# Kernel optimization log

Hardware: AMD Instinct MI355X
Metric: run time of the kernel (lower is better)

## Reference

```python
import jax, jax.numpy as jnp
import numpy as np

BIG = 1000000.0


def setup_inputs() -> dict:
    key = jax.random.key(0)
    k1, k2 = jax.random.split(key)
    embeddings = jax.random.normal(k1, (8192, 128), dtype=jnp.float32)
    labels = jax.random.randint(k2, (8192,), 0, 512, dtype=jnp.int64)
    return {"embeddings": embeddings, "labels": labels, "margin": jnp.float32(0.5)}


def _pairwise_euclidean(x):
    # [N, N] Euclidean distance matrix, numerically safe sqrt (zero diag)
    sq = jnp.sum(x * x, axis=1)
    d2 = sq[:, None] + sq[None, :] - 2.0 * (x @ x.T)
    d2 = jnp.maximum(d2, 0.0)
    nz = d2 > 0.0
    return jnp.where(nz, jnp.sqrt(jnp.where(nz, d2, 1.0)), 0.0)


def reference(embeddings, labels, margin):
    n = embeddings.shape[0]
    dist = _pairwise_euclidean(embeddings)                      # [N, N]
    same = (labels[:, None] == labels[None, :]).astype(dist.dtype)
    mask_pos = same - jnp.eye(n, dtype=dist.dtype)              # positives, excl. self
    mask_neg = 1.0 - same                                       # different label
    pos_dist = jnp.max(dist * mask_pos, axis=1)                 # hardest positive
    neg_dist = jnp.min(dist + (1.0 - mask_neg) * BIG, axis=1)   # hardest negative
    loss = jax.nn.relu(pos_dist - neg_dist + margin)
    return jnp.mean(loss)
```

## Files before the change

### kernel.cpp

```cpp
#include <hip/hip_runtime.h>
#include <hip/hip_bf16.h>

#define NROW 8192
#define DIM  128
#define BI   128
#define BJ   128
#define JSPLIT 8
#define LSTR 136
#define BIGF 1e30f

typedef __attribute__((ext_vector_type(8))) short bf16x8;
typedef __attribute__((ext_vector_type(4))) float f32x4;


__device__ __forceinline__ unsigned short f2bf(float f) {
    unsigned u = __float_as_uint(f);
    unsigned r = (u + 0x7fffu + ((u >> 16) & 1u)) >> 16;
    return (unsigned short)r;
}

__global__ __launch_bounds__(256) void prep_kernel(const float* __restrict__ x,
                                                   unsigned short* __restrict__ xb,
                                                   float* __restrict__ sq,
                                                   unsigned* __restrict__ posb,
                                                   unsigned* __restrict__ negb,
                                                   float* __restrict__ out) {
    int gtid = blockIdx.x * 256 + threadIdx.x;
    if (gtid < NROW) {
        posb[gtid] = 0u;
        negb[gtid] = __float_as_uint(BIGF);
    }
    if (gtid == 0) out[0] = 0.0f;
    int row  = gtid >> 6;
    int lane = threadIdx.x & 63;
    const float* xr = x + (size_t)row * DIM;
    float a = xr[lane];
    float b = xr[lane + 64];
    xb[(size_t)row * DIM + lane]      = f2bf(a);
    xb[(size_t)row * DIM + lane + 64] = f2bf(b);
    float s = a * a + b * b;
    #pragma unroll
    for (int o = 32; o > 0; o >>= 1) s += __shfl_down(s, o);
    if (lane == 0) sq[row] = s;
}

__global__ __launch_bounds__(256, 2) void tri_mfma(const unsigned short* __restrict__ xb,
                                                   const int* __restrict__ lbl,
                                                   const float* __restrict__ sq,
                                                   unsigned* __restrict__ posb,
                                                   unsigned* __restrict__ negb) {
    __shared__ unsigned short As[BI * LSTR];
    __shared__ unsigned short Bs[BJ * LSTR];

    const int bid = blockIdx.x;
    const int rb  = bid >> 3;
    const int jq  = bid & 7;
    const int i0  = rb * BI;
    const int t    = threadIdx.x;
    const int lane = t & 63;
    const int w    = t >> 6;
    const int wrow = (w >> 1) * 64;
    const int wcol = (w & 1) * 64;
    const int quad = lane >> 4;
    const int l15  = lane & 15;

    {
        const int srow = t >> 4;
        const int schk = t & 15;
        #pragma unroll
        for (int it = 0; it < 8; it++) {
            int row = srow + it * 16;
            uint4 v = *(const uint4*)(xb + (size_t)(i0 + row) * DIM + schk * 8);
            *(uint4*)(&As[row * LSTR + schk * 8]) = v;
        }
    }

    float sqi[4][4];
    int   lbli[4][4];
    #pragma unroll
    for (int ti = 0; ti < 4; ti++) {
        int rbase = i0 + wrow + ti * 16 + quad * 4;
        float4 s4 = *(const float4*)(sq + rbase);
        int4   l4 = *(const int4*)(lbl + rbase);
        sqi[ti][0] = s4.x; sqi[ti][1] = s4.y; sqi[ti][2] = s4.z; sqi[ti][3] = s4.w;
        lbli[ti][0] = l4.x; lbli[ti][1] = l4.y; lbli[ti][2] = l4.z; lbli[ti][3] = l4.w;
    }

    float posm[4][4], negm[4][4];
    #pragma unroll
    for (int ti = 0; ti < 4; ti++)
        #pragma unroll
        for (int r = 0; r < 4; r++) { posm[ti][r] = -BIGF; negm[ti][r] = BIGF; }

    #pragma unroll 1
    for (int jt = 0; jt < (NROW / JSPLIT) / BJ; jt++) {
        const int j0 = jq * (NROW / JSPLIT) + jt * BJ;
        __syncthreads();
        {
            const int srow = t >> 4;
            const int schk = t & 15;
            #pragma unroll
            for (int it = 0; it < 8; it++) {
                int row = srow + it * 16;
                uint4 v = *(const uint4*)(xb + (size_t)(j0 + row) * DIM + schk * 8);
                *(uint4*)(&Bs[row * LSTR + schk * 8]) = v;
            }
        }
        __syncthreads();

        float sqj[4]; int lblj[4];
        #pragma unroll
        for (int tj = 0; tj < 4; tj++) {
            int c = j0 + wcol + tj * 16 + l15;
            sqj[tj]  = sq[c];
            lblj[tj] = lbl[c];
        }

        f32x4 acc[4][4];
        #pragma unroll
        for (int ti = 0; ti < 4; ti++)
            #pragma unroll
            for (int tj = 0; tj < 4; tj++) acc[ti][tj] = (f32x4){0.f, 0.f, 0.f, 0.f};

        #pragma unroll
        for (int ks = 0; ks < 4; ks++) {
            bf16x8 af[4], bfr[4];
            #pragma unroll
            for (int ti = 0; ti < 4; ti++)
                af[ti] = *(const bf16x8*)(&As[(wrow + ti * 16 + l15) * LSTR + ks * 32 + quad * 8]);
            #pragma unroll
            for (int tj = 0; tj < 4; tj++)
                bfr[tj] = *(const bf16x8*)(&Bs[(wcol + tj * 16 + l15) * LSTR + ks * 32 + quad * 8]);
            #pragma unroll
            for (int ti = 0; ti < 4; ti++)
                #pragma unroll
                for (int tj = 0; tj < 4; tj++)
                    acc[ti][tj] = __builtin_amdgcn_mfma_f32_16x16x32_bf16(af[ti], bfr[tj], acc[ti][tj], 0, 0, 0);
        }

        const bool diag = (i0 + wrow) == (j0 + wcol);
        #pragma unroll
        for (int ti = 0; ti < 4; ti++)
            #pragma unroll
            for (int tj = 0; tj < 4; tj++)
                #pragma unroll
                for (int r = 0; r < 4; r++) {
                    float s = fmaf(-2.0f, acc[ti][tj][r], sqj[tj]);
                    bool same = (lbli[ti][r] == lblj[tj]);
                    bool isd  = diag && (ti == tj) && (quad * 4 + r == l15);
                    float sp = (same && !isd) ? s : -BIGF;
                    float sn = same ? BIGF : s;
                    posm[ti][r] = fmaxf(posm[ti][r], sp);
                    negm[ti][r] = fminf(negm[ti][r], sn);
                }
    }

    #pragma unroll
    for (int ti = 0; ti < 4; ti++)
        #pragma unroll
        for (int r = 0; r < 4; r++) {
            float p = posm[ti][r];
            float n = negm[ti][r];
            #pragma unroll
            for (int m = 8; m >= 1; m >>= 1) {
                p = fmaxf(p, __shfl_xor(p, m));
                n = fminf(n, __shfl_xor(n, m));
            }
            if (l15 == 0) {
                int row = i0 + wrow + ti * 16 + quad * 4 + r;
                float d2p = fmaxf(0.0f, sqi[ti][r] + p);
                float d2n = fmaxf(0.0f, sqi[ti][r] + n);
                atomicMax(&posb[row], __float_as_uint(d2p));
                atomicMin(&negb[row], __float_as_uint(d2n));
            }
        }
}

__global__ __launch_bounds__(256) void tri_final(const unsigned* __restrict__ posb,
                                                 const unsigned* __restrict__ negb,
                                                 const float* __restrict__ margin,
                                                 float* __restrict__ out) {
    int r = blockIdx.x * 256 + threadIdx.x;
    float m = margin[0];
    float p  = sqrtf(__uint_as_float(posb[r]));
    float ng = sqrtf(__uint_as_float(negb[r]));
    float loss = fmaxf(p - ng + m, 0.0f) * (1.0f / (float)NROW);
    #pragma unroll
    for (int o = 32; o > 0; o >>= 1) loss += __shfl_down(loss, o);
    __shared__ float wsum[4];
    int lane = threadIdx.x & 63, wv = threadIdx.x >> 6;
    if (lane == 0) wsum[wv] = loss;
    __syncthreads();
    if (threadIdx.x == 0) atomicAdd(out, wsum[0] + wsum[1] + wsum[2] + wsum[3]);
}

extern "C" void kernel_launch(void* const* d_in, const int* in_sizes, int n_in,
                              void* d_out, int out_size, void* d_ws, size_t ws_size,
                              hipStream_t stream) {
    const float* x      = (const float*)d_in[0];
    const int*   lbl    = (const int*)d_in[1];
    const float* margin = (const float*)d_in[2];
    float* out = (float*)d_out;

    unsigned short* xb = (unsigned short*)d_ws;
    float*    sq   = (float*)((char*)d_ws + (size_t)NROW * DIM * 2);
    unsigned* posb = (unsigned*)((char*)sq + NROW * 4);
    unsigned* negb = posb + NROW;

    prep_kernel<<<2048, 256, 0, stream>>>(x, xb, sq, posb, negb, out);
    tri_mfma<<<64 * JSPLIT, 256, 0, stream>>>(xb, lbl, sq, posb, negb);
    tri_final<<<NROW / 256, 256, 0, stream>>>(posb, negb, margin, out);
}
```

Measured before the change: 92.10 us.

## Exploit distance symmetry with upper-triangular tile grid and column reductions

Switches from a full 8192x8192 tile sweep (512 blocks each looping over 8 column tiles) to one block per upper-triangular 128x128 tile pair. Each tile now yields both row and column hardest positive and negative via atomics, roughly halving the MFMA work. Global loads go straight into LDS through global_load_lds with an XOR swizzle in place of padding, and A fragments are held in registers. The cost is more atomics, a larger epilogue per tile, and 2080 short blocks that each pay full load latency with no overlap.

```diff
diff --git a/kernel.cpp b/kernel.cpp
--- a/kernel.cpp
+++ b/kernel.cpp
@@ -1,12 +1,10 @@
 #include <hip/hip_runtime.h>
-#include <hip/hip_bf16.h>
 
 #define NROW 8192
 #define DIM  128
 #define BI   128
-#define BJ   128
-#define JSPLIT 8
-#define LSTR 136
+#define NB   (NROW / BI)
+#define NT   (NB * (NB + 1) / 2)
 #define BIGF 1e30f
 
 typedef __attribute__((ext_vector_type(8))) short bf16x8;
@@ -17,6 +15,12 @@
     unsigned u = __float_as_uint(f);
     unsigned r = (u + 0x7fffu + ((u >> 16) & 1u)) >> 16;
     return (unsigned short)r;
+}
+
+__device__ __forceinline__ void gload_lds16(const void* g, void* l) {
+    __builtin_amdgcn_global_load_lds(
+        (const __attribute__((address_space(1))) void*)g,
+        (__attribute__((address_space(3))) void*)l, 16, 0, 0);
 }
 
 __global__ __launch_bounds__(256) void prep_kernel(const float* __restrict__ x,
@@ -49,13 +53,17 @@
                                                    const float* __restrict__ sq,
                                                    unsigned* __restrict__ posb,
                                                    unsigned* __restrict__ negb) {
-    __shared__ unsigned short As[BI * LSTR];
-    __shared__ unsigned short Bs[BJ * LSTR];
+    __shared__ unsigned short As[BI * DIM];
+    __shared__ unsigned short Bs_[BI * DIM];
 
     const int bid = blockIdx.x;
-    const int rb  = bid >> 3;
-    const int jq  = bid & 7;
-    const int i0  = rb * BI;
+    int rb = (int)(64.5f - sqrtf(64.5f * 64.5f - 2.0f * (float)bid));
+    while (rb * NB - rb * (rb - 1) / 2 > bid) rb--;
+    while ((rb + 1) * NB - (rb + 1) * rb / 2 <= bid) rb++;
+    const int cb = rb + (bid - (rb * NB - rb * (rb - 1) / 2));
+    const int i0 = rb * BI;
+    const int j0 = cb * BI;
+
     const int t    = threadIdx.x;
     const int lane = t & 63;
     const int w    = t >> 6;
@@ -64,16 +72,19 @@
     const int quad = lane >> 4;
     const int l15  = lane & 15;
 
-    {
-        const int srow = t >> 4;
-        const int schk = t & 15;
-        #pragma unroll
-        for (int it = 0; it < 8; it++) {
-            int row = srow + it * 16;
-            uint4 v = *(const uint4*)(xb + (size_t)(i0 + row) * DIM + schk * 8);
-            *(uint4*)(&As[row * LSTR + schk * 8]) = v;
-        }
-    }
+    #pragma unroll
+    for (int i = 0; i < 8; i++) {
+        int L    = i * 4096 + t * 16;
+        int row  = L >> 8;
+        int c16s = ((L >> 4) & 15) ^ (row & 7);
+        void* ldst = (char*)As + i * 4096 + w * 1024;
+        gload_lds16(xb + (size_t)(i0 + row) * DIM + c16s * 8, ldst);
+        if (cb != rb) {
+            void* ldstB = (char*)Bs_ + i * 4096 + w * 1024;
+            gload_lds16(xb + (size_t)(j0 + row) * DIM + c16s * 8, ldstB);
+        }
+    }
+    const unsigned short* Bs = (cb == rb) ? As : Bs_;
 
     float sqi[4][4];
     int   lbli[4][4];
@@ -85,75 +96,75 @@
         sqi[ti][0] = s4.x; sqi[ti][1] = s4.y; sqi[ti][2] = s4.z; sqi[ti][3] = s4.w;
         lbli[ti][0] = l4.x; lbli[ti][1] = l4.y; lbli[ti][2] = l4.z; lbli[ti][3] = l4.w;
     }
-
-    float posm[4][4], negm[4][4];
-    #pragma unroll
-    for (int ti = 0; ti < 4; ti++)
-        #pragma unroll
-        for (int r = 0; r < 4; r++) { posm[ti][r] = -BIGF; negm[ti][r] = BIGF; }
-
-    #pragma unroll 1
-    for (int jt = 0; jt < (NROW / JSPLIT) / BJ; jt++) {
-        const int j0 = jq * (NROW / JSPLIT) + jt * BJ;
-        __syncthreads();
-        {
-            const int srow = t >> 4;
-            const int schk = t & 15;
-            #pragma unroll
-            for (int it = 0; it < 8; it++) {
-                int row = srow + it * 16;
-                uint4 v = *(const uint4*)(xb + (size_t)(j0 + row) * DIM + schk * 8);
-                *(uint4*)(&Bs[row * LSTR + schk * 8]) = v;
-            }
-        }
-        __syncthreads();
-
-        float sqj[4]; int lblj[4];
+    float sqj[4]; int lblj[4];
+    #pragma unroll
+    for (int tj = 0; tj < 4; tj++) {
+        int c = j0 + wcol + tj * 16 + l15;
+        sqj[tj]  = sq[c];
+        lblj[tj] = lbl[c];
+    }
+
+    __syncthreads();
+
+    bf16x8 af[4][4];
+    #pragma unroll
+    for (int ti = 0; ti < 4; ti++)
+        #pragma unroll
+        for (int ks = 0; ks < 4; ks++) {
+            int r    = wrow + ti * 16 + l15;
+            int c16s = (ks * 4 + quad) ^ (l15 & 7);
+            af[ti][ks] = *(const bf16x8*)((const char*)As + r * 256 + c16s * 16);
+        }
+
+    f32x4 acc[4][4];
+    #pragma unroll
+    for (int ti = 0; ti < 4; ti++)
+        #pragma unroll
+        for (int tj = 0; tj < 4; tj++) acc[ti][tj] = (f32x4){0.f, 0.f, 0.f, 0.f};
+
+    #pragma unroll
+    for (int ks = 0; ks < 4; ks++) {
+        bf16x8 bfr[4];
         #pragma unroll
         for (int tj = 0; tj < 4; tj++) {
-            int c = j0 + wcol + tj * 16 + l15;
-            sqj[tj]  = sq[c];
-            lblj[tj] = lbl[c];
-        }
-
-        f32x4 acc[4][4];
-        #pragma unroll
-        for (int ti = 0; ti < 4; ti++)
-            #pragma unroll
-            for (int tj = 0; tj < 4; tj++) acc[ti][tj] = (f32x4){0.f, 0.f, 0.f, 0.f};
-
-        #pragma unroll
-        for (int ks = 0; ks < 4; ks++) {
-            bf16x8 af[4], bfr[4];
-            #pragma unroll
-            for (int ti = 0; ti < 4; ti++)
-                af[ti] = *(const bf16x8*)(&As[(wrow + ti * 16 + l15) * LSTR + ks * 32 + quad * 8]);
-            #pragma unroll
-            for (int tj = 0; tj < 4; tj++)
-                bfr[tj] = *(const bf16x8*)(&Bs[(wcol + tj * 16 + l15) * LSTR + ks * 32 + quad * 8]);
-            #pragma unroll
-            for (int ti = 0; ti < 4; ti++)
-                #pragma unroll
-                for (int tj = 0; tj < 4; tj++)
-                    acc[ti][tj] = __builtin_amdgcn_mfma_f32_16x16x32_bf16(af[ti], bfr[tj], acc[ti][tj], 0, 0, 0);
-        }
-
-        const bool diag = (i0 + wrow) == (j0 + wcol);
+            int r    = wcol + tj * 16 + l15;
+            int c16s = (ks * 4 + quad) ^ (l15 & 7);
+            bfr[tj] = *(const bf16x8*)((const char*)Bs + r * 256 + c16s * 16);
+        }
         #pragma unroll
         for (int ti = 0; ti < 4; ti++)
             #pragma unroll
             for (int tj = 0; tj < 4; tj++)
-                #pragma unroll
-                for (int r = 0; r < 4; r++) {
-                    float s = fmaf(-2.0f, acc[ti][tj][r], sqj[tj]);
-                    bool same = (lbli[ti][r] == lblj[tj]);
-                    bool isd  = diag && (ti == tj) && (quad * 4 + r == l15);
-                    float sp = (same && !isd) ? s : -BIGF;
-                    float sn = same ? BIGF : s;
-                    posm[ti][r] = fmaxf(posm[ti][r], sp);
-                    negm[ti][r] = fminf(negm[ti][r], sn);
-                }
-    }
+                acc[ti][tj] = __builtin_amdgcn_mfma_f32_16x16x32_bf16(af[ti][ks], bfr[tj], acc[ti][tj], 0, 0, 0);
+    }
+
+    const bool diag = (rb == cb) && (wrow == wcol);
+    float posm[4][4], negm[4][4];
+    float colp[4], coln[4];
+    #pragma unroll
+    for (int ti = 0; ti < 4; ti++)
+        #pragma unroll
+        for (int r = 0; r < 4; r++) { posm[ti][r] = -BIGF; negm[ti][r] = BIGF; }
+    #pragma unroll
+    for (int tj = 0; tj < 4; tj++) { colp[tj] = -BIGF; coln[tj] = BIGF; }
+
+    #pragma unroll
+    for (int ti = 0; ti < 4; ti++)
+        #pragma unroll
+        for (int tj = 0; tj < 4; tj++)
+            #pragma unroll
+            for (int r = 0; r < 4; r++) {
+                float d  = acc[ti][tj][r];
+                float sr = fmaf(-2.0f, d, sqj[tj]);
+                float sc = fmaf(-2.0f, d, sqi[ti][r]);
+                bool same = (lbli[ti][r] == lblj[tj]);
+                bool isd  = diag && (ti == tj) && (quad * 4 + r == l15);
+                bool okp  = same && !isd;
+                posm[ti][r] = fmaxf(posm[ti][r], okp  ? sr : -BIGF);
+                negm[ti][r] = fminf(negm[ti][r], same ? BIGF : sr);
+                colp[tj]    = fmaxf(colp[tj],    okp  ? sc : -BIGF);
+                coln[tj]    = fminf(coln[tj],    same ? BIGF : sc);
+            }
 
     #pragma unroll
     for (int ti = 0; ti < 4; ti++)
@@ -174,6 +185,23 @@
                 atomicMin(&negb[row], __float_as_uint(d2n));
             }
         }
+
+    #pragma unroll
+    for (int tj = 0; tj < 4; tj++) {
+        float p = colp[tj];
+        float n = coln[tj];
+        p = fmaxf(p, __shfl_xor(p, 16));
+        p = fmaxf(p, __shfl_xor(p, 32));
+        n = fminf(n, __shfl_xor(n, 16));
+        n = fminf(n, __shfl_xor(n, 32));
+        if (quad == 0) {
+            int col = j0 + wcol + tj * 16 + l15;
+            float d2p = fmaxf(0.0f, sqj[tj] + p);
+            float d2n = fmaxf(0.0f, sqj[tj] + n);
+            atomicMax(&posb[col], __float_as_uint(d2p));
+            atomicMin(&negb[col], __float_as_uint(d2n));
+        }
+    }
 }
 
 __global__ __launch_bounds__(256) void tri_final(const unsigned* __restrict__ posb,
@@ -208,6 +236,6 @@
     unsigned* negb = posb + NROW;
 
     prep_kernel<<<2048, 256, 0, stream>>>(x, xb, sq, posb, negb, out);
-    tri_mfma<<<64 * JSPLIT, 256, 0, stream>>>(xb, lbl, sq, posb, negb);
+    tri_mfma<<<NT, 256, 0, stream>>>(xb, lbl, sq, posb, negb);
     tri_final<<<NROW / 256, 256, 0, stream>>>(posb, negb, margin, out);
 }
```

Measured after the change: 118.3 us. 28.4% more time.

## Pre-swizzle bf16 tiles, double-buffer B via direct global-to-LDS loads, drop atomics

Applied to the files above, without the earlier changes.

The prep kernel writes the bf16 embeddings in a 16-row blocked layout so tiles can be streamed straight into LDS with global_load_lds. The main kernel keeps A fragments in registers, double-buffers 64-column B tiles in LDS, and splits the columns into 16 segments with smaller per-wave tiles to reach more occupancy. Per-row atomics are replaced by per-segment partial buffers that the final kernel reduces. This aims to hide the B-tile load latency and remove atomic contention, in exchange for a narrower per-wave MFMA tile and more blocks reloading the same data.

```diff
diff --git a/kernel.cpp b/kernel.cpp
--- a/kernel.cpp
+++ b/kernel.cpp
@@ -1,12 +1,8 @@
 #include <hip/hip_runtime.h>
-#include <hip/hip_bf16.h>
 
 #define NROW 8192
 #define DIM  128
-#define BI   128
-#define BJ   128
-#define JSPLIT 8
-#define LSTR 136
+#define NSEG 16
 #define BIGF 1e30f
 
 typedef __attribute__((ext_vector_type(8))) short bf16x8;
@@ -19,144 +15,144 @@
     return (unsigned short)r;
 }
 
+__device__ __forceinline__ void gload_lds16(const void* g, void* l) {
+    __builtin_amdgcn_global_load_lds(
+        (const __attribute__((address_space(1))) void*)g,
+        (__attribute__((address_space(3))) void*)l, 16, 0, 0);
+}
+
 __global__ __launch_bounds__(256) void prep_kernel(const float* __restrict__ x,
-                                                   unsigned short* __restrict__ xb,
+                                                   unsigned short* __restrict__ xb2,
                                                    float* __restrict__ sq,
-                                                   unsigned* __restrict__ posb,
-                                                   unsigned* __restrict__ negb,
                                                    float* __restrict__ out) {
     int gtid = blockIdx.x * 256 + threadIdx.x;
-    if (gtid < NROW) {
-        posb[gtid] = 0u;
-        negb[gtid] = __float_as_uint(BIGF);
-    }
     if (gtid == 0) out[0] = 0.0f;
     int row  = gtid >> 6;
     int lane = threadIdx.x & 63;
     const float* xr = x + (size_t)row * DIM;
     float a = xr[lane];
     float b = xr[lane + 64];
-    xb[(size_t)row * DIM + lane]      = f2bf(a);
-    xb[(size_t)row * DIM + lane + 64] = f2bf(b);
+    size_t d0 = (size_t)(row >> 4) * 2048 + (size_t)(lane >> 3) * 128
+              + (size_t)(row & 15) * 8 + (lane & 7);
+    xb2[d0]            = f2bf(a);
+    xb2[d0 + 8 * 128]  = f2bf(b);
     float s = a * a + b * b;
     #pragma unroll
     for (int o = 32; o > 0; o >>= 1) s += __shfl_down(s, o);
     if (lane == 0) sq[row] = s;
 }
 
-__global__ __launch_bounds__(256, 2) void tri_mfma(const unsigned short* __restrict__ xb,
-                                                   const int* __restrict__ lbl,
-                                                   const float* __restrict__ sq,
-                                                   unsigned* __restrict__ posb,
-                                                   unsigned* __restrict__ negb) {
-    __shared__ unsigned short As[BI * LSTR];
-    __shared__ unsigned short Bs[BJ * LSTR];
-
+__global__ __launch_bounds__(256, 3) void tile_mfma(const unsigned short* __restrict__ xb2,
+                                                    const int* __restrict__ lbl,
+                                                    const float* __restrict__ sq,
+                                                    float* __restrict__ posS,
+                                                    float* __restrict__ negS) {
+    __shared__ unsigned short Bs[2][64 * DIM];
     const int bid = blockIdx.x;
-    const int rb  = bid >> 3;
-    const int jq  = bid & 7;
-    const int i0  = rb * BI;
+    const int rb  = bid >> 4;
+    const int jq  = bid & 15;
+    const int i0  = rb * 128;
+    const int jbase = jq * 512;
     const int t    = threadIdx.x;
     const int lane = t & 63;
     const int w    = t >> 6;
-    const int wrow = (w >> 1) * 64;
-    const int wcol = (w & 1) * 64;
+    const int wr0  = i0 + w * 32;
     const int quad = lane >> 4;
     const int l15  = lane & 15;
 
+    const char* xbB = (const char*)xb2;
+
+    bf16x8 af[2][4];
+    const int gA = wr0 >> 4;
+    #pragma unroll
+    for (int ti = 0; ti < 2; ti++)
+        #pragma unroll
+        for (int ks = 0; ks < 4; ks++)
+            af[ti][ks] = *(const bf16x8*)(xb2 + (size_t)(gA + ti) * 2048 + (ks * 4 + quad) * 128 + l15 * 8);
+
+    int lbli[2][4];
+    #pragma unroll
+    for (int ti = 0; ti < 2; ti++) {
+        int4 l4 = *(const int4*)(lbl + wr0 + ti * 16 + quad * 4);
+        lbli[ti][0] = l4.x; lbli[ti][1] = l4.y; lbli[ti][2] = l4.z; lbli[ti][3] = l4.w;
+    }
+    const bool hasDiag = (i0 >= jbase) && (i0 < jbase + 512);
+
+    float posm[2][4], negm[2][4];
+    #pragma unroll
+    for (int ti = 0; ti < 2; ti++)
+        #pragma unroll
+        for (int r = 0; r < 4; r++) { posm[ti][r] = -BIGF; negm[ti][r] = BIGF; }
+
     {
-        const int srow = t >> 4;
-        const int schk = t & 15;
-        #pragma unroll
-        for (int it = 0; it < 8; it++) {
-            int row = srow + it * 16;
-            uint4 v = *(const uint4*)(xb + (size_t)(i0 + row) * DIM + schk * 8);
-            *(uint4*)(&As[row * LSTR + schk * 8]) = v;
-        }
-    }
-
-    float sqi[4][4];
-    int   lbli[4][4];
-    #pragma unroll
-    for (int ti = 0; ti < 4; ti++) {
-        int rbase = i0 + wrow + ti * 16 + quad * 4;
-        float4 s4 = *(const float4*)(sq + rbase);
-        int4   l4 = *(const int4*)(lbl + rbase);
-        sqi[ti][0] = s4.x; sqi[ti][1] = s4.y; sqi[ti][2] = s4.z; sqi[ti][3] = s4.w;
-        lbli[ti][0] = l4.x; lbli[ti][1] = l4.y; lbli[ti][2] = l4.z; lbli[ti][3] = l4.w;
-    }
-
-    float posm[4][4], negm[4][4];
-    #pragma unroll
-    for (int ti = 0; ti < 4; ti++)
-        #pragma unroll
-        for (int r = 0; r < 4; r++) { posm[ti][r] = -BIGF; negm[ti][r] = BIGF; }
+        const char* src = xbB + (size_t)(jbase >> 4) * 4096;
+        #pragma unroll
+        for (int i = 0; i < 4; i++)
+            gload_lds16(src + i * 4096 + t * 16, (char*)&Bs[0][0] + i * 4096 + w * 1024);
+    }
+    __syncthreads();
 
     #pragma unroll 1
-    for (int jt = 0; jt < (NROW / JSPLIT) / BJ; jt++) {
-        const int j0 = jq * (NROW / JSPLIT) + jt * BJ;
-        __syncthreads();
-        {
-            const int srow = t >> 4;
-            const int schk = t & 15;
-            #pragma unroll
-            for (int it = 0; it < 8; it++) {
-                int row = srow + it * 16;
-                uint4 v = *(const uint4*)(xb + (size_t)(j0 + row) * DIM + schk * 8);
-                *(uint4*)(&Bs[row * LSTR + schk * 8]) = v;
-            }
-        }
-        __syncthreads();
+    for (int jt = 0; jt < 8; jt++) {
+        const int cur = jt & 1;
+        const int j0  = jbase + jt * 64;
+
+        if (jt < 7) {
+            const char* src = xbB + (size_t)((j0 + 64) >> 4) * 4096;
+            #pragma unroll
+            for (int i = 0; i < 4; i++)
+                gload_lds16(src + i * 4096 + t * 16, (char*)&Bs[cur ^ 1][0] + i * 4096 + w * 1024);
+        }
 
         float sqj[4]; int lblj[4];
         #pragma unroll
         for (int tj = 0; tj < 4; tj++) {
-            int c = j0 + wcol + tj * 16 + l15;
+            int c = j0 + tj * 16 + l15;
             sqj[tj]  = sq[c];
             lblj[tj] = lbl[c];
         }
 
-        f32x4 acc[4][4];
-        #pragma unroll
-        for (int ti = 0; ti < 4; ti++)
+        f32x4 acc[2][4];
+        #pragma unroll
+        for (int ti = 0; ti < 2; ti++)
             #pragma unroll
             for (int tj = 0; tj < 4; tj++) acc[ti][tj] = (f32x4){0.f, 0.f, 0.f, 0.f};
 
         #pragma unroll
         for (int ks = 0; ks < 4; ks++) {
-            bf16x8 af[4], bfr[4];
-            #pragma unroll
-            for (int ti = 0; ti < 4; ti++)
-                af[ti] = *(const bf16x8*)(&As[(wrow + ti * 16 + l15) * LSTR + ks * 32 + quad * 8]);
+            bf16x8 bfr[4];
             #pragma unroll
             for (int tj = 0; tj < 4; tj++)
-                bfr[tj] = *(const bf16x8*)(&Bs[(wcol + tj * 16 + l15) * LSTR + ks * 32 + quad * 8]);
-            #pragma unroll
-            for (int ti = 0; ti < 4; ti++)
+                bfr[tj] = *(const bf16x8*)((const char*)&Bs[cur][0] + tj * 4096 + (ks * 4 + quad) * 256 + l15 * 16);
+            #pragma unroll
+            for (int ti = 0; ti < 2; ti++)
                 #pragma unroll
                 for (int tj = 0; tj < 4; tj++)
-                    acc[ti][tj] = __builtin_amdgcn_mfma_f32_16x16x32_bf16(af[ti], bfr[tj], acc[ti][tj], 0, 0, 0);
-        }
-
-        const bool diag = (i0 + wrow) == (j0 + wcol);
-        #pragma unroll
-        for (int ti = 0; ti < 4; ti++)
-            #pragma unroll
-            for (int tj = 0; tj < 4; tj++)
+                    acc[ti][tj] = __builtin_amdgcn_mfma_f32_16x16x32_bf16(af[ti][ks], bfr[tj], acc[ti][tj], 0, 0, 0);
+        }
+
+        #pragma unroll
+        for (int ti = 0; ti < 2; ti++) {
+            const int rowg = wr0 + ti * 16 + quad * 4;
+            #pragma unroll
+            for (int tj = 0; tj < 4; tj++) {
+                const int jc = j0 + tj * 16 + l15;
                 #pragma unroll
                 for (int r = 0; r < 4; r++) {
-                    float s = fmaf(-2.0f, acc[ti][tj][r], sqj[tj]);
+                    float sr = fmaf(-2.0f, acc[ti][tj][r], sqj[tj]);
                     bool same = (lbli[ti][r] == lblj[tj]);
-                    bool isd  = diag && (ti == tj) && (quad * 4 + r == l15);
-                    float sp = (same && !isd) ? s : -BIGF;
-                    float sn = same ? BIGF : s;
-                    posm[ti][r] = fmaxf(posm[ti][r], sp);
-                    negm[ti][r] = fminf(negm[ti][r], sn);
+                    bool self = hasDiag && (jc == rowg + r);
+                    posm[ti][r] = fmaxf(posm[ti][r], (same && !self) ? sr : -BIGF);
+                    negm[ti][r] = fminf(negm[ti][r], same ? BIGF : sr);
                 }
-    }
-
-    #pragma unroll
-    for (int ti = 0; ti < 4; ti++)
+            }
+        }
+
+        __syncthreads();
+    }
+
+    #pragma unroll
+    for (int ti = 0; ti < 2; ti++)
         #pragma unroll
         for (int r = 0; r < 4; r++) {
             float p = posm[ti][r];
@@ -167,24 +163,27 @@
                 n = fminf(n, __shfl_xor(n, m));
             }
             if (l15 == 0) {
-                int row = i0 + wrow + ti * 16 + quad * 4 + r;
-                float d2p = fmaxf(0.0f, sqi[ti][r] + p);
-                float d2n = fmaxf(0.0f, sqi[ti][r] + n);
-                atomicMax(&posb[row], __float_as_uint(d2p));
-                atomicMin(&negb[row], __float_as_uint(d2n));
+                int row = wr0 + ti * 16 + quad * 4 + r;
+                float sqi = sq[row];
+                posS[jq * NROW + row] = fmaxf(0.0f, sqi + p);
+                negS[jq * NROW + row] = fmaxf(0.0f, sqi + n);
             }
         }
 }
 
-__global__ __launch_bounds__(256) void tri_final(const unsigned* __restrict__ posb,
-                                                 const unsigned* __restrict__ negb,
+__global__ __launch_bounds__(256) void tri_final(const float* __restrict__ posS,
+                                                 const float* __restrict__ negS,
                                                  const float* __restrict__ margin,
                                                  float* __restrict__ out) {
     int r = blockIdx.x * 256 + threadIdx.x;
+    float p = 0.0f, n = BIGF;
+    #pragma unroll
+    for (int q = 0; q < NSEG; q++) {
+        p = fmaxf(p, posS[q * NROW + r]);
+        n = fminf(n, negS[q * NROW + r]);
+    }
     float m = margin[0];
-    float p  = sqrtf(__uint_as_float(posb[r]));
-    float ng = sqrtf(__uint_as_float(negb[r]));
-    float loss = fmaxf(p - ng + m, 0.0f) * (1.0f / (float)NROW);
+    float loss = fmaxf(sqrtf(p) - sqrtf(n) + m, 0.0f) * (1.0f / (float)NROW);
     #pragma unroll
     for (int o = 32; o > 0; o >>= 1) loss += __shfl_down(loss, o);
     __shared__ float wsum[4];
@@ -202,12 +201,13 @@
     const float* margin = (const float*)d_in[2];
     float* out = (float*)d_out;
 
-    unsigned short* xb = (unsigned short*)d_ws;
-    float*    sq   = (float*)((char*)d_ws + (size_t)NROW * DIM * 2);
-    unsigned* posb = (unsigned*)((char*)sq + NROW * 4);
-    unsigned* negb = posb + NROW;
-
-    prep_kernel<<<2048, 256, 0, stream>>>(x, xb, sq, posb, negb, out);
-    tri_mfma<<<64 * JSPLIT, 256, 0, stream>>>(xb, lbl, sq, posb, negb);
-    tri_final<<<NROW / 256, 256, 0, stream>>>(posb, negb, margin, out);
-}
+    char* ws = (char*)d_ws;
+    unsigned short* xb2 = (unsigned short*)ws;
+    float* sq   = (float*)(ws + (2u << 20));
+    float* posS = (float*)(ws + (2u << 20) + (64u << 10));
+    float* negS = (float*)(ws + (2u << 20) + (576u << 10));
+
+    prep_kernel<<<2048, 256, 0, stream>>>(x, xb2, sq, out);
+    tile_mfma<<<64 * NSEG, 256, 0, stream>>>(xb2, lbl, sq, posS, negS);
+    tri_final<<<NROW / 256, 256, 0, stream>>>(posS, negS, margin, out);
+}
```

After: 90.08 us. -2.2%, faster.
